# Performance work log

Hardware: AMD Instinct MI355X
Metric: run time of the kernel (lower is better)

## Reference

```python
import jax, jax.numpy as jnp
import numpy as np


def setup_inputs() -> dict:
    key = jax.random.key(0)
    ks = jax.random.split(key, 4)
    B, T, D, H = 128, 512, 256, 512
    scale = 1.0 / np.sqrt(D)
    return {
        "x": jax.random.normal(ks[0], (B, T, D), dtype=jnp.float32),
        "h0": jnp.zeros((B, H), dtype=jnp.float32),
        "kernelr": jax.random.normal(ks[1], (D, H), dtype=jnp.float32) * scale,
        "kernelz": jax.random.normal(ks[2], (D, H), dtype=jnp.float32) * scale,
        "kernelh": jax.random.normal(ks[3], (D, H), dtype=jnp.float32) * scale,
        "memoryr": jnp.ones((H,), dtype=jnp.float32),
        "memoryz": jnp.ones((H,), dtype=jnp.float32),
        "br": jnp.zeros((H,), dtype=jnp.float32),
        "bz": jnp.zeros((H,), dtype=jnp.float32),
    }


def reference(x, h0, kernelr, kernelz, kernelh, memoryr, memoryz, br, bz):
    # Precompute all input projections as one batched GEMM over (B*T, D).
    # xr/xz/xh: [T, B, H]
    xr = jnp.einsum("btd,dh->tbh", x, kernelr) + br
    xz = jnp.einsum("btd,dh->tbh", x, kernelz) + bz
    xh = jnp.einsum("btd,dh->tbh", x, kernelh)

    def step(h, inp):
        pr, pz, ph = inp
        r = jnp.tanh(pr + h * memoryr) + 1.0
        z = jax.nn.sigmoid(pz + h * memoryz)
        out = z * h + (1.0 - z) * jnp.tanh(ph + r * h)
        return out, out

    _, outs = jax.lax.scan(step, h0, (xr, xz, xh))  # outs: [T, B, H]
    return jnp.transpose(outs, (1, 0, 2))  # [B, T, H]
```

## Files before the change

### kernel.cpp

```cpp
#include <hip/hip_runtime.h>

typedef _Float16 f16;
typedef _Float16 f16x8 __attribute__((ext_vector_type(8)));
typedef _Float16 f16x4 __attribute__((ext_vector_type(4)));
typedef float f32x4 __attribute__((ext_vector_type(4)));

__device__ __forceinline__ float rcpf(float x) { return __builtin_amdgcn_rcpf(x); }

__device__ __forceinline__ void gload_lds16(const void* g, void* l) {
  __builtin_amdgcn_global_load_lds(
      (const __attribute__((address_space(1))) void*)g,
      (__attribute__((address_space(3))) void*)l, 16, 0, 0);
}

__global__ void __launch_bounds__(256) cvt_w(const float* __restrict__ Wr,
                                             const float* __restrict__ Wz,
                                             const float* __restrict__ Wh,
                                             f16* __restrict__ out) {
  int o = blockIdx.x * 256 + threadIdx.x;
  int rl = o & 15, ni = (o >> 4) & 3, kq = (o >> 6) & 3, kt = (o >> 8) & 7;
  int wnt = o >> 11;
  int w = wnt % 3, nt = wnt / 3;
  int n = nt * 64 + ni * 16 + rl;
  int k0 = kt * 32 + kq * 8;
  const float* W = (w == 0) ? Wr : ((w == 1) ? Wz : Wh);
  f16x8 v;
#pragma unroll
  for (int e = 0; e < 8; ++e) v[e] = (f16)W[(size_t)(k0 + e) * 512 + n];
  *(f16x8*)(out + (size_t)o * 8) = v;
}

__global__ void __launch_bounds__(256) cvt_x(const float* __restrict__ in,
                                             f16* __restrict__ out) {
  int o = blockIdx.x * 256 + threadIdx.x;
  int rl = o & 15, kq = (o >> 4) & 3, kt = (o >> 6) & 7, m16 = o >> 9;
  const float* src = in + (size_t)(m16 * 16 + rl) * 256 + kt * 32 + kq * 8;
  f16x8 v;
#pragma unroll
  for (int e = 0; e < 8; ++e) v[e] = (f16)src[e];
  *(f16x8*)(out + (size_t)o * 8) = v;
}

__global__ void __launch_bounds__(512, 4) brc_fused(
    const f16* __restrict__ Af, const f16* __restrict__ Bf,
    const float* __restrict__ h0, const float* __restrict__ mr,
    const float* __restrict__ mz, const float* __restrict__ br,
    const float* __restrict__ bz, float* __restrict__ out) {
  __shared__ __align__(16) f16 Pl[2][12288];
  __shared__ __align__(16) f16 Al[8192];
  const int tid = threadIdx.x;
  const int wid = tid >> 6, lane = tid & 63;
  const int bid = blockIdx.x;
  const int lid = (bid & 7) * 64 + (bid >> 3);
  const int b = lid >> 2, hs = lid & 3;

  const int w3 = wid >> 1, hh = wid & 1;
  const int nt = hs * 2 + hh;
  const char* Bp = (const char*)Bf + (lane >> 4) * 1024 + (lane & 15) * 16 +
                   (size_t)(nt * 3 + w3) * 32768;
  const int col = lane & 15, rbase = (lane >> 4) * 4;

  const int c = tid & 127;
  const int hg = hs * 128 + c;
  float h = h0[(size_t)b * 512 + hg];
  const float mrc = 2.0f * mr[hg], mzc = -mz[hg];
  const float br2 = 2.0f * br[hg], nbz = -bz[hg];

#define STAGEA(q)                                                             \
  do {                                                                        \
    const char* gsrc = (const char*)Af + ((size_t)(b * 32 + (q) * 2) * 8) * 1024; \
    for (int j = wid; j < 16; j += 6)                                         \
      gload_lds16(gsrc + (size_t)j * 1024 + lane * 16, (char*)Al + j * 1024); \
  } while (0)

  auto gemm_phase = [&](int q) {
    f16* Pb = Pl[q & 1];
    f32x4 acc[2][4] = {};
#pragma unroll
    for (int kt = 0; kt < 8; ++kt) {
      f16x8 a[2], bfr[4];
#pragma unroll
      for (int mi = 0; mi < 2; ++mi)
        a[mi] = *(const f16x8*)((const char*)Al + (mi * 8 + kt) * 1024 + lane * 16);
#pragma unroll
      for (int ni = 0; ni < 4; ++ni)
        bfr[ni] = *(const f16x8*)(Bp + (size_t)kt * 4096 + ni * 256);
#pragma unroll
      for (int mi = 0; mi < 2; ++mi)
#pragma unroll
        for (int ni = 0; ni < 4; ++ni)
          acc[mi][ni] = __builtin_amdgcn_mfma_f32_16x16x32_f16(
              a[mi], bfr[ni], acc[mi][ni], 0, 0, 0);
    }
#pragma unroll
    for (int mi = 0; mi < 2; ++mi) {
      int tl = mi * 16 + rbase;
#pragma unroll
      for (int ni = 0; ni < 4; ++ni) {
        int hl = hh * 64 + ni * 16 + col;
        f16x4 v;
#pragma unroll
        for (int r = 0; r < 4; ++r) v[r] = (f16)acc[mi][ni][r];
        *(f16x4*)&Pb[w3 * 4096 + (tl >> 3) * 1024 + hl * 8 + (tl & 7)] = v;
      }
    }
  };

  if (wid < 6) STAGEA(0);
  __syncthreads();
  if (wid < 6) gemm_phase(0);

  for (int p = 0; p < 16; ++p) {
    __syncthreads();
    if (wid < 6 && p + 1 < 16) STAGEA(p + 1);
    __syncthreads();
    if (wid < 6) {
      if (p + 1 < 16) gemm_phase(p + 1);
    } else {
      const f16* Pr_ = &Pl[p & 1][c * 8];
      const f16* Pz_ = Pr_ + 4096;
      const f16* Ph_ = Pr_ + 8192;
      float* opm = out + ((size_t)b * 512 + p * 32) * 512 + hg;
#pragma unroll
      for (int g = 0; g < 4; ++g) {
        f16x8 R  = *(const f16x8*)(Pr_ + g * 1024);
        f16x8 Z  = *(const f16x8*)(Pz_ + g * 1024);
        f16x8 Hh = *(const f16x8*)(Ph_ + g * 1024);
#pragma unroll
        for (int j = 0; j < 8; ++j) {
          float prs = fmaf((float)R[j], 2.0f, br2);
          float pzs = fmaf((float)Z[j], -1.0f, nbz);
          float ph2 = (float)Hh[j] * 2.0f;
          float er = __expf(fmaf(h, mrc, prs));
          float rr = fmaf(-2.0f, rcpf(er + 1.0f), 2.0f);
          float ez = __expf(fmaf(h, mzc, pzs));
          float zz = rcpf(1.0f + ez);
          float ec = __expf(fmaf(rr, h + h, ph2));
          float cd = fmaf(-2.0f, rcpf(ec + 1.0f), 1.0f);
          h = fmaf(zz, h - cd, cd);
          __builtin_nontemporal_store(h, opm + (size_t)(g * 8 + j) * 512);
        }
      }
    }
  }
#undef STAGEA
}

extern "C" void kernel_launch(void* const* d_in, const int* in_sizes, int n_in,
                              void* d_out, int out_size, void* d_ws, size_t ws_size,
                              hipStream_t stream) {
  const float* x  = (const float*)d_in[0];
  const float* h0 = (const float*)d_in[1];
  const float* kr = (const float*)d_in[2];
  const float* kz = (const float*)d_in[3];
  const float* kh = (const float*)d_in[4];
  const float* mr = (const float*)d_in[5];
  const float* mz = (const float*)d_in[6];
  const float* br = (const float*)d_in[7];
  const float* bz = (const float*)d_in[8];
  float* out = (float*)d_out;

  f16* Bf = (f16*)d_ws;
  f16* Xf = Bf + 393216;

  cvt_w<<<192, 256, 0, stream>>>(kr, kz, kh, Bf);
  cvt_x<<<8192, 256, 0, stream>>>(x, Xf);
  brc_fused<<<512, 512, 0, stream>>>(Xf, Bf, h0, mr, mz, br, bz, out);
}
```

Measured before the change: 110.4 us.

## Fuse x fp32-to-fp16 conversion into fused GEMM-scan kernel with swizzled LDS

Drops the separate cvt_x kernel that wrote a repacked fp16 copy of x. The fused kernel now streams fp32 x rows straight into LDS with an XOR swizzle and converts to fp16 while loading MFMA A-fragments. This removes one kernel launch and a full write and reread of the x copy. In exchange it doubles the LDS footprint and global bytes per A stage and adds conversion work inside the GEMM warps.

```diff
diff --git a/kernel.cpp b/kernel.cpp
--- a/kernel.cpp
+++ b/kernel.cpp
@@ -30,24 +30,13 @@
   *(f16x8*)(out + (size_t)o * 8) = v;
 }
 
-__global__ void __launch_bounds__(256) cvt_x(const float* __restrict__ in,
-                                             f16* __restrict__ out) {
-  int o = blockIdx.x * 256 + threadIdx.x;
-  int rl = o & 15, kq = (o >> 4) & 3, kt = (o >> 6) & 7, m16 = o >> 9;
-  const float* src = in + (size_t)(m16 * 16 + rl) * 256 + kt * 32 + kq * 8;
-  f16x8 v;
-#pragma unroll
-  for (int e = 0; e < 8; ++e) v[e] = (f16)src[e];
-  *(f16x8*)(out + (size_t)o * 8) = v;
-}
-
 __global__ void __launch_bounds__(512, 4) brc_fused(
-    const f16* __restrict__ Af, const f16* __restrict__ Bf,
+    const float* __restrict__ X32, const f16* __restrict__ Bf,
     const float* __restrict__ h0, const float* __restrict__ mr,
     const float* __restrict__ mz, const float* __restrict__ br,
     const float* __restrict__ bz, float* __restrict__ out) {
   __shared__ __align__(16) f16 Pl[2][12288];
-  __shared__ __align__(16) f16 Al[8192];
+  __shared__ __align__(16) float Alf[8192];
   const int tid = threadIdx.x;
   const int wid = tid >> 6, lane = tid & 63;
   const int bid = blockIdx.x;
@@ -59,6 +48,7 @@
   const char* Bp = (const char*)Bf + (lane >> 4) * 1024 + (lane & 15) * 16 +
                    (size_t)(nt * 3 + w3) * 32768;
   const int col = lane & 15, rbase = (lane >> 4) * 4;
+  const char* Xb = (const char*)(X32 + (size_t)b * 131072);
 
   const int c = tid & 127;
   const int hg = hs * 128 + c;
@@ -68,20 +58,33 @@
 
 #define STAGEA(q)                                                             \
   do {                                                                        \
-    const char* gsrc = (const char*)Af + ((size_t)(b * 32 + (q) * 2) * 8) * 1024; \
-    for (int j = wid; j < 16; j += 6)                                         \
-      gload_lds16(gsrc + (size_t)j * 1024 + lane * 16, (char*)Al + j * 1024); \
+    for (int j = wid; j < 32; j += 6)                                         \
+      gload_lds16(Xb + (size_t)((q) * 32 + j) * 1024 +                        \
+                      ((lane * 16) ^ ((j & 7) << 4)),                         \
+                  (char*)Alf + j * 1024);                                     \
   } while (0)
 
   auto gemm_phase = [&](int q) {
     f16* Pb = Pl[q & 1];
     f32x4 acc[2][4] = {};
+    const int rl = lane & 15, kq = lane >> 4;
 #pragma unroll
     for (int kt = 0; kt < 8; ++kt) {
       f16x8 a[2], bfr[4];
 #pragma unroll
-      for (int mi = 0; mi < 2; ++mi)
-        a[mi] = *(const f16x8*)((const char*)Al + (mi * 8 + kt) * 1024 + lane * 16);
+      for (int mi = 0; mi < 2; ++mi) {
+        int row = mi * 16 + rl;
+        int off = kt * 128 + kq * 32;
+        int s = (row & 7) << 4;
+        const char* base = (const char*)Alf + row * 1024;
+        f32x4 lo = *(const f32x4*)(base + ((off) ^ s));
+        f32x4 hi = *(const f32x4*)(base + ((off + 16) ^ s));
+#pragma unroll
+        for (int e = 0; e < 4; ++e) {
+          a[mi][e] = (f16)lo[e];
+          a[mi][4 + e] = (f16)hi[e];
+        }
+      }
 #pragma unroll
       for (int ni = 0; ni < 4; ++ni)
         bfr[ni] = *(const f16x8*)(Bp + (size_t)kt * 4096 + ni * 256);
@@ -161,9 +164,7 @@
   float* out = (float*)d_out;
 
   f16* Bf = (f16*)d_ws;
-  f16* Xf = Bf + 393216;
 
   cvt_w<<<192, 256, 0, stream>>>(kr, kz, kh, Bf);
-  cvt_x<<<8192, 256, 0, stream>>>(x, Xf);
-  brc_fused<<<512, 512, 0, stream>>>(Xf, Bf, h0, mr, mz, br, bz, out);
+  brc_fused<<<512, 512, 0, stream>>>(x, Bf, h0, mr, mz, br, bz, out);
 }
```

Result: slower. 132.9 us (+20.4%).
